# Kernel optimization log

Measured on AMD Instinct MI355X. Metric: run time of the kernel, lower is better.

Reference implementation:

```python
import jax, jax.numpy as jnp
import numpy as np

N = 100000   # nodes
D = 64       # padded neighbor-list width (avg degree)
F = 256      # in_channels
H = 256      # hidden_channels
E = 131072   # number of target edges
OUT = 1      # out_channels


def _linear_params(key, fin, fout):
    k1, k2 = jax.random.split(key)
    s = 1.0 / np.sqrt(fin)
    w = jax.random.uniform(k1, (fin, fout), jnp.float32, -s, s)
    b = jax.random.uniform(k2, (fout,), jnp.float32, -s, s)
    return w, b


def setup_inputs() -> dict:
    key = jax.random.key(0)
    ks = jax.random.split(key, 12)
    x = jax.random.normal(ks[0], (N, F), jnp.float32)
    # sorted padded neighbor lists: row i -> D neighbor ids (sorted, as in the
    # bit-packed sorted-element representation the torch code intersects)
    neighbors = jnp.sort(jax.random.randint(ks[1], (N, D), 0, N), axis=1).astype(jnp.int32)
    tar_ei = jax.random.randint(ks[2], (2, E), 0, N).astype(jnp.int32)
    cn_w1, cn_b1 = _linear_params(ks[3], 1, H)
    cn_w2, cn_b2 = _linear_params(ks[4], H, H)
    cn_w3, cn_b3 = _linear_params(ks[5], H, H)
    ij_w1, ij_b1 = _linear_params(ks[6], F, H)
    ij_w2, ij_b2 = _linear_params(ks[7], H, H)
    lin_w1, lin_b1 = _linear_params(ks[8], H, H)
    lin_w2, lin_b2 = _linear_params(ks[9], H, OUT)
    beta = jnp.ones((1,), jnp.float32)
    return dict(x=x, neighbors=neighbors, tar_ei=tar_ei, beta=beta,
                cn_w1=cn_w1, cn_b1=cn_b1, cn_w2=cn_w2, cn_b2=cn_b2,
                cn_w3=cn_w3, cn_b3=cn_b3,
                ij_w1=ij_w1, ij_b1=ij_b1, ij_w2=ij_w2, ij_b2=ij_b2,
                lin_w1=lin_w1, lin_b1=lin_b1, lin_w2=lin_w2, lin_b2=lin_b2)


def reference(x, neighbors, tar_ei, beta,
              cn_w1, cn_b1, cn_w2, cn_b2, cn_w3, cn_b3,
              ij_w1, ij_b1, ij_w2, ij_b2,
              lin_w1, lin_b1, lin_w2, lin_b2):
    src, dst = tar_ei[0], tar_ei[1]
    xi = x[src]                       # [E, F] irregular gather
    xj = x[dst]                       # [E, F]

    # adjoverlap / spmoverlap_: per edge, |N(i) ∩ N(j)| via sorted-set
    # intersection; cn.sum(dim=-1) with fill value 1.0 -> CN count.
    ni = neighbors[src]               # [E, D]
    nj = neighbors[dst]               # [E, D]
    matches = ni[:, :, None] == nj[:, None, :]          # [E, D, D]
    xcn = jnp.sum(matches, axis=(1, 2)).astype(jnp.float32)[:, None]  # [E, 1]

    # xcnlin: Linear(1,H) -> ReLU -> Linear(H,H) -> ReLU -> Linear(H,H)
    h = jax.nn.relu(xcn @ cn_w1 + cn_b1)
    h = jax.nn.relu(h @ cn_w2 + cn_b2)
    xcn_feat = h @ cn_w3 + cn_b3                         # [E, H]

    # xijlin: Linear(F,H) -> ReLU -> Linear(H,H)
    g = jax.nn.relu((xi * xj) @ ij_w1 + ij_b1)
    xij = g @ ij_w2 + ij_b2                              # [E, H]

    # lin: Linear(H,H) -> ReLU -> Linear(H,OUT)
    z = jax.nn.relu((xcn_feat * beta + xij) @ lin_w1 + lin_b1)
    out = z @ lin_w2 + lin_b2                            # [E, OUT]
    return out
```

## Files before the change

### kernel.cpp

```cpp
#include <hip/hip_runtime.h>
#include <hip/hip_bf16.h>
#include <stdint.h>

#define EE 131072
#define DDEG 64

typedef __bf16 bf16_t;
typedef bf16_t bf16x8 __attribute__((ext_vector_type(8)));
typedef float floatx4 __attribute__((ext_vector_type(4)));

__global__ __launch_bounds__(256)
void cn_kernel(const int* __restrict__ nbr, const int* __restrict__ tar,
               int* __restrict__ xcn) {
    int wid  = (blockIdx.x * 256 + threadIdx.x) >> 6;
    int lane = threadIdx.x & 63;
    int s = __builtin_amdgcn_readfirstlane(tar[wid]);
    int d = __builtin_amdgcn_readfirstlane(tar[EE + wid]);
    int a = nbr[(size_t)s * DDEG + lane];
    const int* __restrict__ brow = nbr + (size_t)d * DDEG;
    int cnt = 0;
    #pragma unroll
    for (int k = 0; k < 64; ++k)
        cnt += __builtin_popcountll(__ballot(a == brow[k]));
    if (lane == 0) xcn[wid] = cnt;
}

__global__ __launch_bounds__(256)
void prep_kernel(const float* __restrict__ x, bf16_t* __restrict__ xb,
                 const float* __restrict__ ij_w1, bf16_t* __restrict__ Wt1,
                 const float* __restrict__ w2, const float* __restrict__ lw1,
                 bf16_t* __restrict__ Mt,
                 const float* __restrict__ b2, const float* __restrict__ lb1,
                 float* __restrict__ cvec,
                 const float* __restrict__ cw1, const float* __restrict__ cb1,
                 const float* __restrict__ cw2, const float* __restrict__ cb2,
                 const float* __restrict__ cw3, const float* __restrict__ cb3,
                 const float* __restrict__ beta, float* __restrict__ T2) {
    __shared__ __align__(16) char arena[33792];
    const int bid = blockIdx.x;
    const int t = threadIdx.x;

    if (bid >= 1088) {
        size_t base = (size_t)(bid - 1088) * 4096 + (size_t)t * 16;
        float4 a0 = *(const float4*)(x + base);
        float4 a1 = *(const float4*)(x + base + 4);
        float4 a2 = *(const float4*)(x + base + 8);
        float4 a3 = *(const float4*)(x + base + 12);
        bf16x8 o0, o1;
        o0[0] = (bf16_t)a0.x; o0[1] = (bf16_t)a0.y; o0[2] = (bf16_t)a0.z; o0[3] = (bf16_t)a0.w;
        o0[4] = (bf16_t)a1.x; o0[5] = (bf16_t)a1.y; o0[6] = (bf16_t)a1.z; o0[7] = (bf16_t)a1.w;
        o1[0] = (bf16_t)a2.x; o1[1] = (bf16_t)a2.y; o1[2] = (bf16_t)a2.z; o1[3] = (bf16_t)a2.w;
        o1[4] = (bf16_t)a3.x; o1[5] = (bf16_t)a3.y; o1[6] = (bf16_t)a3.z; o1[7] = (bf16_t)a3.w;
        *(bf16x8*)(xb + base)     = o0;
        *(bf16x8*)(xb + base + 8) = o1;
        return;
    }

    if (bid < 64) {
        float (*tile)[33] = (float (*)[33])arena;
        int bx = bid & 7, by = bid >> 3;
        int tx = t & 31, ty = t >> 5;
        #pragma unroll
        for (int r = 0; r < 32; r += 8)
            tile[ty + r][tx] = ij_w1[(by * 32 + ty + r) * 256 + bx * 32 + tx];
        __syncthreads();
        #pragma unroll
        for (int r = 0; r < 32; r += 8)
            Wt1[(bx * 32 + ty + r) * 256 + by * 32 + tx] = (bf16_t)tile[tx][ty + r];
    } else if (bid < 320) {
        float (*S)[33] = (float (*)[33])arena;
        int b = bid - 64;
        int cc = t & 31, abase = t >> 5;
        float acc = 0.f;
        for (int c0 = 0; c0 < 256; c0 += 32) {
            __syncthreads();
            #pragma unroll
            for (int r = 0; r < 32; ++r) {
                int a = r * 8 + abase;
                S[a][cc] = w2[a * 256 + c0 + cc];
            }
            __syncthreads();
            #pragma unroll 8
            for (int c2 = 0; c2 < 32; ++c2) {
                float wv = lw1[(c0 + c2) * 256 + b];
                acc += S[t][c2] * wv;
            }
        }
        Mt[(size_t)b * 256 + t] = (bf16_t)acc;
    } else if (bid < 576) {
        float* red = (float*)arena;
        int b = bid - 320;
        red[t] = b2[t] * lw1[t * 256 + b];
        __syncthreads();
        for (int s = 128; s > 0; s >>= 1) {
            if (t < s) red[t] += red[t + s];
            __syncthreads();
        }
        if (t == 0) cvec[b] = red[0] + lb1[b];
    } else {
        float* t1 = (float*)arena;
        float* t2 = (float*)(arena + 1024);
        float* t3 = (float*)(arena + 2048);
        int v = bid - 576;
        float fv = (float)v;
        t1[t] = fmaxf(fv * cw1[t] + cb1[t], 0.f);
        __syncthreads();
        float s = cb2[t];
        for (int k = 0; k < 256; ++k) s += t1[k] * cw2[k * 256 + t];
        t2[t] = fmaxf(s, 0.f);
        __syncthreads();
        s = cb3[t];
        for (int k = 0; k < 256; ++k) s += t2[k] * cw3[k * 256 + t];
        t3[t] = s * beta[0];
        __syncthreads();
        s = 0.f;
        for (int k = 0; k < 256; ++k) s += t3[k] * lw1[k * 256 + t];
        T2[(size_t)v * 256 + t] = s;
    }
}

__global__ __launch_bounds__(256, 4)
void fused_kernel(const bf16_t* __restrict__ xb, const int* __restrict__ tar,
                  const bf16_t* __restrict__ Wt1, const float* __restrict__ b1,
                  const bf16_t* __restrict__ Mt, const float* __restrict__ cvec,
                  const float* __restrict__ T2, const int* __restrict__ xcn,
                  const float* __restrict__ w2, const float* __restrict__ b2s,
                  float* __restrict__ out) {
    __shared__ __align__(16) bf16_t X[64 * 264];
    __shared__ float rowacc[64];

    const int tid  = threadIdx.x;
    const int lane = tid & 63;
    const int wc   = tid >> 6;
    const int quad = lane >> 4;
    const int l16  = lane & 15;
    const int e0   = blockIdx.x * 64;

    {
        const int srow   = tid >> 2;
        const int skbase = (tid & 3) * 8;
        int e = e0 + srow;
        const bf16_t* xi = xb + (size_t)tar[e] * 256 + skbase;
        const bf16_t* xj = xb + (size_t)tar[EE + e] * 256 + skbase;
        bf16x8 ui[8], vj[8];
        #pragma unroll
        for (int kc = 0; kc < 8; ++kc) {
            ui[kc] = *(const bf16x8*)(xi + kc * 32);
            vj[kc] = *(const bf16x8*)(xj + kc * 32);
        }
        #pragma unroll
        for (int kc = 0; kc < 8; ++kc) {
            bf16x8 p;
            #pragma unroll
            for (int m = 0; m < 8; ++m)
                p[m] = (bf16_t)((float)ui[kc][m] * (float)vj[kc][m]);
            *(bf16x8*)&X[srow * 264 + kc * 32 + skbase] = p;
        }
    }

    floatx4 acc[4][4];
    #pragma unroll
    for (int i = 0; i < 4; ++i)
        #pragma unroll
        for (int j = 0; j < 4; ++j)
            acc[i][j] = (floatx4){0.f, 0.f, 0.f, 0.f};

    __syncthreads();

    #pragma unroll 2
    for (int kc = 0; kc < 8; ++kc) {
        const int k0 = kc * 32 + quad * 8;
        bf16x8 af[4], bfr[4];
        #pragma unroll
        for (int j = 0; j < 4; ++j)
            bfr[j] = *(const bf16x8*)(Wt1 + (size_t)(wc * 64 + j * 16 + l16) * 256 + k0);
        #pragma unroll
        for (int i = 0; i < 4; ++i)
            af[i] = *(const bf16x8*)(&X[(i * 16 + l16) * 264 + k0]);
        #pragma unroll
        for (int i = 0; i < 4; ++i)
            #pragma unroll
            for (int j = 0; j < 4; ++j)
                acc[i][j] = __builtin_amdgcn_mfma_f32_16x16x32_bf16(
                                af[i], bfr[j], acc[i][j], 0, 0, 0);
    }

    __syncthreads();

    #pragma unroll
    for (int j = 0; j < 4; ++j) {
        int col  = wc * 64 + j * 16 + l16;
        float bv = b1[col];
        #pragma unroll
        for (int i = 0; i < 4; ++i)
            #pragma unroll
            for (int r = 0; r < 4; ++r) {
                int row = i * 16 + quad * 4 + r;
                X[row * 264 + col] = (bf16_t)fmaxf(acc[i][j][r] + bv, 0.f);
            }
    }
    #pragma unroll
    for (int i = 0; i < 4; ++i)
        #pragma unroll
        for (int j = 0; j < 4; ++j)
            acc[i][j] = (floatx4){0.f, 0.f, 0.f, 0.f};
    if (tid < 64) rowacc[tid] = 0.f;

    __syncthreads();

    #pragma unroll 2
    for (int kc = 0; kc < 8; ++kc) {
        const int k0 = kc * 32 + quad * 8;
        bf16x8 af[4], bfr[4];
        #pragma unroll
        for (int j = 0; j < 4; ++j)
            bfr[j] = *(const bf16x8*)(Mt + (size_t)(wc * 64 + j * 16 + l16) * 256 + k0);
        #pragma unroll
        for (int i = 0; i < 4; ++i)
            af[i] = *(const bf16x8*)(&X[(i * 16 + l16) * 264 + k0]);
        #pragma unroll
        for (int i = 0; i < 4; ++i)
            #pragma unroll
            for (int j = 0; j < 4; ++j)
                acc[i][j] = __builtin_amdgcn_mfma_f32_16x16x32_bf16(
                                af[i], bfr[j], acc[i][j], 0, 0, 0);
    }

    int xv[16];
    #pragma unroll
    for (int i = 0; i < 4; ++i)
        #pragma unroll
        for (int r = 0; r < 4; ++r) {
            int v = xcn[e0 + i * 16 + quad * 4 + r];
            xv[i * 4 + r] = v < 511 ? v : 511;
        }

    float pr[16];
    #pragma unroll
    for (int t = 0; t < 16; ++t) pr[t] = 0.f;
    #pragma unroll
    for (int j = 0; j < 4; ++j) {
        int col  = wc * 64 + j * 16 + l16;
        float cv = cvec[col];
        float wv = w2[col];
        #pragma unroll
        for (int i = 0; i < 4; ++i)
            #pragma unroll
            for (int r = 0; r < 4; ++r) {
                float t2v = T2[(size_t)xv[i * 4 + r] * 256 + col];
                float v = fmaxf(acc[i][j][r] + cv + t2v, 0.f);
                pr[i * 4 + r] += v * wv;
            }
    }
    #pragma unroll
    for (int off = 1; off < 16; off <<= 1)
        #pragma unroll
        for (int t = 0; t < 16; ++t)
            pr[t] += __shfl_xor(pr[t], off, 64);
    if (l16 == 0) {
        #pragma unroll
        for (int i = 0; i < 4; ++i)
            #pragma unroll
            for (int r = 0; r < 4; ++r)
                atomicAdd(&rowacc[i * 16 + quad * 4 + r], pr[i * 4 + r]);
    }
    __syncthreads();
    if (tid < 64) out[e0 + tid] = rowacc[tid] + b2s[0];
}

extern "C" void kernel_launch(void* const* d_in, const int* in_sizes, int n_in,
                              void* d_out, int out_size, void* d_ws, size_t ws_size,
                              hipStream_t stream) {
    const float* x      = (const float*)d_in[0];
    const int*   nbr    = (const int*)  d_in[1];
    const int*   tar    = (const int*)  d_in[2];
    const float* beta   = (const float*)d_in[3];
    const float* cn_w1  = (const float*)d_in[4];
    const float* cn_b1  = (const float*)d_in[5];
    const float* cn_w2  = (const float*)d_in[6];
    const float* cn_b2  = (const float*)d_in[7];
    const float* cn_w3  = (const float*)d_in[8];
    const float* cn_b3  = (const float*)d_in[9];
    const float* ij_w1  = (const float*)d_in[10];
    const float* ij_b1  = (const float*)d_in[11];
    const float* ij_w2  = (const float*)d_in[12];
    const float* ij_b2  = (const float*)d_in[13];
    const float* lin_w1 = (const float*)d_in[14];
    const float* lin_b1 = (const float*)d_in[15];
    const float* lin_w2 = (const float*)d_in[16];
    const float* lin_b2 = (const float*)d_in[17];

    char* ws = (char*)d_ws;
    float*  T2    = (float*) (ws + 0);
    int*    xcn   = (int*)   (ws + 524288);
    bf16_t* Wt1   = (bf16_t*)(ws + 1048576);
    bf16_t* Mt    = (bf16_t*)(ws + 1179648);
    float*  cvec  = (float*) (ws + 1310720);
    bf16_t* xb    = (bf16_t*)(ws + 1312768);

    cn_kernel<<<EE / 4, 256, 0, stream>>>(nbr, tar, xcn);
    prep_kernel<<<1088 + 6250, 256, 0, stream>>>(
        x, xb, ij_w1, Wt1, ij_w2, lin_w1, Mt,
        ij_b2, lin_b1, cvec,
        cn_w1, cn_b1, cn_w2, cn_b2, cn_w3, cn_b3, beta, T2);
    fused_kernel<<<EE / 64, 256, 0, stream>>>(xb, tar, Wt1, ij_b1, Mt, cvec,
                                              T2, xcn, lin_w2, lin_b2,
                                              (float*)d_out);
}
```

Baseline: 371.0 us.

## Fuse common-neighbor count into MLP kernel with binary-search intersection and swizzled LDS

Removes the separate cn_kernel and computes the common-neighbor count inside the fused MLP kernel, dropping a global round trip for xcn and one launch. The count now uses a per-lane binary search over shuffled sorted neighbor lists (lower/upper bound) in place of 64 ballots. The edge tile shrinks from 64 to 32 rows per block and occupancy is raised to 6 blocks. LDS padding is replaced by an XOR swizzle to avoid bank conflicts. Smaller tiles mean the weight fragments (Wt1, Mt) are reloaded from memory twice as often per edge.

```diff
diff --git a/kernel.cpp b/kernel.cpp
--- a/kernel.cpp
+++ b/kernel.cpp
@@ -9,21 +9,7 @@
 typedef bf16_t bf16x8 __attribute__((ext_vector_type(8)));
 typedef float floatx4 __attribute__((ext_vector_type(4)));
 
-__global__ __launch_bounds__(256)
-void cn_kernel(const int* __restrict__ nbr, const int* __restrict__ tar,
-               int* __restrict__ xcn) {
-    int wid  = (blockIdx.x * 256 + threadIdx.x) >> 6;
-    int lane = threadIdx.x & 63;
-    int s = __builtin_amdgcn_readfirstlane(tar[wid]);
-    int d = __builtin_amdgcn_readfirstlane(tar[EE + wid]);
-    int a = nbr[(size_t)s * DDEG + lane];
-    const int* __restrict__ brow = nbr + (size_t)d * DDEG;
-    int cnt = 0;
-    #pragma unroll
-    for (int k = 0; k < 64; ++k)
-        cnt += __builtin_popcountll(__ballot(a == brow[k]));
-    if (lane == 0) xcn[wid] = cnt;
-}
+#define SWZ(row, k) (((row) << 8) + ((k) ^ (((row) & 7) << 3)))
 
 __global__ __launch_bounds__(256)
 void prep_kernel(const float* __restrict__ x, bf16_t* __restrict__ xb,
@@ -119,48 +105,77 @@
     }
 }
 
-__global__ __launch_bounds__(256, 4)
+__global__ __launch_bounds__(256, 6)
 void fused_kernel(const bf16_t* __restrict__ xb, const int* __restrict__ tar,
+                  const int* __restrict__ nbr,
                   const bf16_t* __restrict__ Wt1, const float* __restrict__ b1,
                   const bf16_t* __restrict__ Mt, const float* __restrict__ cvec,
-                  const float* __restrict__ T2, const int* __restrict__ xcn,
+                  const float* __restrict__ T2,
                   const float* __restrict__ w2, const float* __restrict__ b2s,
                   float* __restrict__ out) {
-    __shared__ __align__(16) bf16_t X[64 * 264];
-    __shared__ float rowacc[64];
+    __shared__ __align__(16) bf16_t X[32 * 256];
+    __shared__ float rowacc[32];
+    __shared__ int xcn_s[32];
 
     const int tid  = threadIdx.x;
     const int lane = tid & 63;
     const int wc   = tid >> 6;
     const int quad = lane >> 4;
     const int l16  = lane & 15;
-    const int e0   = blockIdx.x * 64;
+    const int e0   = blockIdx.x * 32;
 
     {
-        const int srow   = tid >> 2;
-        const int skbase = (tid & 3) * 8;
+        const int srow   = tid >> 3;
+        const int skbase = (tid & 7) * 8;
         int e = e0 + srow;
         const bf16_t* xi = xb + (size_t)tar[e] * 256 + skbase;
         const bf16_t* xj = xb + (size_t)tar[EE + e] * 256 + skbase;
-        bf16x8 ui[8], vj[8];
-        #pragma unroll
-        for (int kc = 0; kc < 8; ++kc) {
-            ui[kc] = *(const bf16x8*)(xi + kc * 32);
-            vj[kc] = *(const bf16x8*)(xj + kc * 32);
-        }
-        #pragma unroll
-        for (int kc = 0; kc < 8; ++kc) {
+        bf16x8 ui[4], vj[4];
+        #pragma unroll
+        for (int kc = 0; kc < 4; ++kc) {
+            ui[kc] = *(const bf16x8*)(xi + kc * 64);
+            vj[kc] = *(const bf16x8*)(xj + kc * 64);
+        }
+        #pragma unroll
+        for (int kc = 0; kc < 4; ++kc) {
             bf16x8 p;
             #pragma unroll
             for (int m = 0; m < 8; ++m)
                 p[m] = (bf16_t)((float)ui[kc][m] * (float)vj[kc][m]);
-            *(bf16x8*)&X[srow * 264 + kc * 32 + skbase] = p;
-        }
-    }
-
-    floatx4 acc[4][4];
-    #pragma unroll
-    for (int i = 0; i < 4; ++i)
+            *(bf16x8*)&X[SWZ(srow, kc * 64 + skbase)] = p;
+        }
+    }
+
+    #pragma unroll 2
+    for (int i = 0; i < 8; ++i) {
+        int e = e0 + wc * 8 + i;
+        int s = __builtin_amdgcn_readfirstlane(tar[e]);
+        int d = __builtin_amdgcn_readfirstlane(tar[EE + e]);
+        int va = nbr[(size_t)s * DDEG + lane];
+        int vb = nbr[(size_t)d * DDEG + lane];
+        int lo = 0, hi = 0;
+        #pragma unroll
+        for (int st = 32; st; st >>= 1) {
+            int bv = __shfl(vb, lo + st - 1, 64);
+            lo += (bv < va) ? st : 0;
+        }
+        #pragma unroll
+        for (int st = 32; st; st >>= 1) {
+            int bv = __shfl(vb, hi + st - 1, 64);
+            hi += (bv <= va) ? st : 0;
+        }
+        int b63 = __shfl(vb, 63, 64);
+        lo += (b63 < va) ? 1 : 0;
+        hi += (b63 <= va) ? 1 : 0;
+        int c = hi - lo;
+        #pragma unroll
+        for (int off = 32; off; off >>= 1) c += __shfl_xor(c, off, 64);
+        if (lane == 0) xcn_s[wc * 8 + i] = (c < 511) ? c : 511;
+    }
+
+    floatx4 acc[2][4];
+    #pragma unroll
+    for (int i = 0; i < 2; ++i)
         #pragma unroll
         for (int j = 0; j < 4; ++j)
             acc[i][j] = (floatx4){0.f, 0.f, 0.f, 0.f};
@@ -170,15 +185,17 @@
     #pragma unroll 2
     for (int kc = 0; kc < 8; ++kc) {
         const int k0 = kc * 32 + quad * 8;
-        bf16x8 af[4], bfr[4];
+        bf16x8 af[2], bfr[4];
         #pragma unroll
         for (int j = 0; j < 4; ++j)
             bfr[j] = *(const bf16x8*)(Wt1 + (size_t)(wc * 64 + j * 16 + l16) * 256 + k0);
         #pragma unroll
-        for (int i = 0; i < 4; ++i)
-            af[i] = *(const bf16x8*)(&X[(i * 16 + l16) * 264 + k0]);
-        #pragma unroll
-        for (int i = 0; i < 4; ++i)
+        for (int i = 0; i < 2; ++i) {
+            int row = i * 16 + l16;
+            af[i] = *(const bf16x8*)(&X[SWZ(row, k0)]);
+        }
+        #pragma unroll
+        for (int i = 0; i < 2; ++i)
             #pragma unroll
             for (int j = 0; j < 4; ++j)
                 acc[i][j] = __builtin_amdgcn_mfma_f32_16x16x32_bf16(
@@ -192,59 +209,59 @@
         int col  = wc * 64 + j * 16 + l16;
         float bv = b1[col];
         #pragma unroll
-        for (int i = 0; i < 4; ++i)
+        for (int i = 0; i < 2; ++i)
             #pragma unroll
             for (int r = 0; r < 4; ++r) {
                 int row = i * 16 + quad * 4 + r;
-                X[row * 264 + col] = (bf16_t)fmaxf(acc[i][j][r] + bv, 0.f);
+                X[SWZ(row, col)] = (bf16_t)fmaxf(acc[i][j][r] + bv, 0.f);
             }
     }
     #pragma unroll
-    for (int i = 0; i < 4; ++i)
+    for (int i = 0; i < 2; ++i)
         #pragma unroll
         for (int j = 0; j < 4; ++j)
             acc[i][j] = (floatx4){0.f, 0.f, 0.f, 0.f};
-    if (tid < 64) rowacc[tid] = 0.f;
+    if (tid < 32) rowacc[tid] = 0.f;
 
     __syncthreads();
 
     #pragma unroll 2
     for (int kc = 0; kc < 8; ++kc) {
         const int k0 = kc * 32 + quad * 8;
-        bf16x8 af[4], bfr[4];
+        bf16x8 af[2], bfr[4];
         #pragma unroll
         for (int j = 0; j < 4; ++j)
             bfr[j] = *(const bf16x8*)(Mt + (size_t)(wc * 64 + j * 16 + l16) * 256 + k0);
         #pragma unroll
-        for (int i = 0; i < 4; ++i)
-            af[i] = *(const bf16x8*)(&X[(i * 16 + l16) * 264 + k0]);
-        #pragma unroll
-        for (int i = 0; i < 4; ++i)
+        for (int i = 0; i < 2; ++i) {
+            int row = i * 16 + l16;
+            af[i] = *(const bf16x8*)(&X[SWZ(row, k0)]);
+        }
+        #pragma unroll
+        for (int i = 0; i < 2; ++i)
             #pragma unroll
             for (int j = 0; j < 4; ++j)
                 acc[i][j] = __builtin_amdgcn_mfma_f32_16x16x32_bf16(
                                 af[i], bfr[j], acc[i][j], 0, 0, 0);
     }
 
-    int xv[16];
-    #pragma unroll
-    for (int i = 0; i < 4; ++i)
-        #pragma unroll
-        for (int r = 0; r < 4; ++r) {
-            int v = xcn[e0 + i * 16 + quad * 4 + r];
-            xv[i * 4 + r] = v < 511 ? v : 511;
-        }
-
-    float pr[16];
-    #pragma unroll
-    for (int t = 0; t < 16; ++t) pr[t] = 0.f;
+    int xv[8];
+    #pragma unroll
+    for (int i = 0; i < 2; ++i)
+        #pragma unroll
+        for (int r = 0; r < 4; ++r)
+            xv[i * 4 + r] = xcn_s[i * 16 + quad * 4 + r];
+
+    float pr[8];
+    #pragma unroll
+    for (int t = 0; t < 8; ++t) pr[t] = 0.f;
     #pragma unroll
     for (int j = 0; j < 4; ++j) {
         int col  = wc * 64 + j * 16 + l16;
         float cv = cvec[col];
         float wv = w2[col];
         #pragma unroll
-        for (int i = 0; i < 4; ++i)
+        for (int i = 0; i < 2; ++i)
             #pragma unroll
             for (int r = 0; r < 4; ++r) {
                 float t2v = T2[(size_t)xv[i * 4 + r] * 256 + col];
@@ -255,17 +272,17 @@
     #pragma unroll
     for (int off = 1; off < 16; off <<= 1)
         #pragma unroll
-        for (int t = 0; t < 16; ++t)
+        for (int t = 0; t < 8; ++t)
             pr[t] += __shfl_xor(pr[t], off, 64);
     if (l16 == 0) {
         #pragma unroll
-        for (int i = 0; i < 4; ++i)
+        for (int i = 0; i < 2; ++i)
             #pragma unroll
             for (int r = 0; r < 4; ++r)
                 atomicAdd(&rowacc[i * 16 + quad * 4 + r], pr[i * 4 + r]);
     }
     __syncthreads();
-    if (tid < 64) out[e0 + tid] = rowacc[tid] + b2s[0];
+    if (tid < 32) out[e0 + tid] = rowacc[tid] + b2s[0];
 }
 
 extern "C" void kernel_launch(void* const* d_in, const int* in_sizes, int n_in,
@@ -292,18 +309,16 @@
 
     char* ws = (char*)d_ws;
     float*  T2    = (float*) (ws + 0);
-    int*    xcn   = (int*)   (ws + 524288);
     bf16_t* Wt1   = (bf16_t*)(ws + 1048576);
     bf16_t* Mt    = (bf16_t*)(ws + 1179648);
     float*  cvec  = (float*) (ws + 1310720);
     bf16_t* xb    = (bf16_t*)(ws + 1312768);
 
-    cn_kernel<<<EE / 4, 256, 0, stream>>>(nbr, tar, xcn);
     prep_kernel<<<1088 + 6250, 256, 0, stream>>>(
         x, xb, ij_w1, Wt1, ij_w2, lin_w1, Mt,
         ij_b2, lin_b1, cvec,
         cn_w1, cn_b1, cn_w2, cn_b2, cn_w3, cn_b3, beta, T2);
-    fused_kernel<<<EE / 64, 256, 0, stream>>>(xb, tar, Wt1, ij_b1, Mt, cvec,
-                                              T2, xcn, lin_w2, lin_b2,
+    fused_kernel<<<EE / 32, 256, 0, stream>>>(xb, tar, nbr, Wt1, ij_b1, Mt, cvec,
+                                              T2, lin_w2, lin_b2,
                                               (float*)d_out);
 }
```

New measurement: 389.3 us. 4.9% more time.

## Fuse common-neighbor counting into main kernel via binary-search intersection and swizzle LDS

Applied to the files above, without the earlier changes.

Removes the separate cn_kernel and computes per-edge common-neighbor counts inside fused_kernel. Each wave loads both neighbor rows and counts matches per element with a shuffle-based binary search over the sorted partner row, replacing 64 ballots. Counts are packed two per int for the reduction and stored in LDS. The X tile drops its padding and uses an XOR swizzle to avoid bank conflicts. Launch bounds go from 4 to 3 blocks per CU, since the 32 extra registers holding neighbor rows raise register pressure and lower occupancy.

```diff
diff --git a/kernel.cpp b/kernel.cpp
--- a/kernel.cpp
+++ b/kernel.cpp
@@ -9,21 +9,7 @@
 typedef bf16_t bf16x8 __attribute__((ext_vector_type(8)));
 typedef float floatx4 __attribute__((ext_vector_type(4)));
 
-__global__ __launch_bounds__(256)
-void cn_kernel(const int* __restrict__ nbr, const int* __restrict__ tar,
-               int* __restrict__ xcn) {
-    int wid  = (blockIdx.x * 256 + threadIdx.x) >> 6;
-    int lane = threadIdx.x & 63;
-    int s = __builtin_amdgcn_readfirstlane(tar[wid]);
-    int d = __builtin_amdgcn_readfirstlane(tar[EE + wid]);
-    int a = nbr[(size_t)s * DDEG + lane];
-    const int* __restrict__ brow = nbr + (size_t)d * DDEG;
-    int cnt = 0;
-    #pragma unroll
-    for (int k = 0; k < 64; ++k)
-        cnt += __builtin_popcountll(__ballot(a == brow[k]));
-    if (lane == 0) xcn[wid] = cnt;
-}
+#define SWZ(row, k) (((row) << 8) + ((k) ^ (((row) & 7) << 3)))
 
 __global__ __launch_bounds__(256)
 void prep_kernel(const float* __restrict__ x, bf16_t* __restrict__ xb,
@@ -119,15 +105,17 @@
     }
 }
 
-__global__ __launch_bounds__(256, 4)
+__global__ __launch_bounds__(256, 3)
 void fused_kernel(const bf16_t* __restrict__ xb, const int* __restrict__ tar,
+                  const int* __restrict__ nbr,
                   const bf16_t* __restrict__ Wt1, const float* __restrict__ b1,
                   const bf16_t* __restrict__ Mt, const float* __restrict__ cvec,
-                  const float* __restrict__ T2, const int* __restrict__ xcn,
+                  const float* __restrict__ T2,
                   const float* __restrict__ w2, const float* __restrict__ b2s,
                   float* __restrict__ out) {
-    __shared__ __align__(16) bf16_t X[64 * 264];
+    __shared__ __align__(16) bf16_t X[64 * 256];
     __shared__ float rowacc[64];
+    __shared__ int xcn_s[64];
 
     const int tid  = threadIdx.x;
     const int lane = tid & 63;
@@ -135,6 +123,16 @@
     const int quad = lane >> 4;
     const int l16  = lane & 15;
     const int e0   = blockIdx.x * 64;
+
+    int va[16], vb[16];
+    #pragma unroll
+    for (int i = 0; i < 16; ++i) {
+        int e = e0 + wc * 16 + i;
+        int s = __builtin_amdgcn_readfirstlane(tar[e]);
+        int d = __builtin_amdgcn_readfirstlane(tar[EE + e]);
+        va[i] = nbr[(size_t)s * DDEG + lane];
+        vb[i] = nbr[(size_t)d * DDEG + lane];
+    }
 
     {
         const int srow   = tid >> 2;
@@ -154,7 +152,37 @@
             #pragma unroll
             for (int m = 0; m < 8; ++m)
                 p[m] = (bf16_t)((float)ui[kc][m] * (float)vj[kc][m]);
-            *(bf16x8*)&X[srow * 264 + kc * 32 + skbase] = p;
+            *(bf16x8*)&X[SWZ(srow, kc * 32 + skbase)] = p;
+        }
+    }
+
+    __syncthreads();
+
+    #pragma unroll
+    for (int p = 0; p < 8; ++p) {
+        int cpk = 0;
+        #pragma unroll
+        for (int h = 0; h < 2; ++h) {
+            int i = p * 2 + h;
+            int lo = 0, hi = 0;
+            #pragma unroll
+            for (int st = 32; st; st >>= 1) {
+                int bl = __shfl(vb[i], lo + st - 1, 64);
+                int bh = __shfl(vb[i], hi + st - 1, 64);
+                lo += (bl < va[i]) ? st : 0;
+                hi += (bh <= va[i]) ? st : 0;
+            }
+            int b63 = __shfl(vb[i], 63, 64);
+            lo += (b63 < va[i]) ? 1 : 0;
+            hi += (b63 <= va[i]) ? 1 : 0;
+            cpk += (hi - lo) << (16 * h);
+        }
+        #pragma unroll
+        for (int off = 32; off; off >>= 1) cpk += __shfl_xor(cpk, off, 64);
+        if (lane == 0) {
+            int c0 = cpk & 0xffff, c1 = (int)((unsigned)cpk >> 16);
+            xcn_s[wc * 16 + p * 2]     = c0 < 511 ? c0 : 511;
+            xcn_s[wc * 16 + p * 2 + 1] = c1 < 511 ? c1 : 511;
         }
     }
 
@@ -164,8 +192,6 @@
         #pragma unroll
         for (int j = 0; j < 4; ++j)
             acc[i][j] = (floatx4){0.f, 0.f, 0.f, 0.f};
-
-    __syncthreads();
 
     #pragma unroll 2
     for (int kc = 0; kc < 8; ++kc) {
@@ -176,7 +202,7 @@
             bfr[j] = *(const bf16x8*)(Wt1 + (size_t)(wc * 64 + j * 16 + l16) * 256 + k0);
         #pragma unroll
         for (int i = 0; i < 4; ++i)
-            af[i] = *(const bf16x8*)(&X[(i * 16 + l16) * 264 + k0]);
+            af[i] = *(const bf16x8*)(&X[SWZ(i * 16 + l16, k0)]);
         #pragma unroll
         for (int i = 0; i < 4; ++i)
             #pragma unroll
@@ -196,7 +222,7 @@
             #pragma unroll
             for (int r = 0; r < 4; ++r) {
                 int row = i * 16 + quad * 4 + r;
-                X[row * 264 + col] = (bf16_t)fmaxf(acc[i][j][r] + bv, 0.f);
+                X[SWZ(row, col)] = (bf16_t)fmaxf(acc[i][j][r] + bv, 0.f);
             }
     }
     #pragma unroll
@@ -217,7 +243,7 @@
             bfr[j] = *(const bf16x8*)(Mt + (size_t)(wc * 64 + j * 16 + l16) * 256 + k0);
         #pragma unroll
         for (int i = 0; i < 4; ++i)
-            af[i] = *(const bf16x8*)(&X[(i * 16 + l16) * 264 + k0]);
+            af[i] = *(const bf16x8*)(&X[SWZ(i * 16 + l16, k0)]);
         #pragma unroll
         for (int i = 0; i < 4; ++i)
             #pragma unroll
@@ -230,10 +256,8 @@
     #pragma unroll
     for (int i = 0; i < 4; ++i)
         #pragma unroll
-        for (int r = 0; r < 4; ++r) {
-            int v = xcn[e0 + i * 16 + quad * 4 + r];
-            xv[i * 4 + r] = v < 511 ? v : 511;
-        }
+        for (int r = 0; r < 4; ++r)
+            xv[i * 4 + r] = xcn_s[i * 16 + quad * 4 + r];
 
     float pr[16];
     #pragma unroll
@@ -292,18 +316,16 @@
 
     char* ws = (char*)d_ws;
     float*  T2    = (float*) (ws + 0);
-    int*    xcn   = (int*)   (ws + 524288);
     bf16_t* Wt1   = (bf16_t*)(ws + 1048576);
     bf16_t* Mt    = (bf16_t*)(ws + 1179648);
     float*  cvec  = (float*) (ws + 1310720);
     bf16_t* xb    = (bf16_t*)(ws + 1312768);
 
-    cn_kernel<<<EE / 4, 256, 0, stream>>>(nbr, tar, xcn);
     prep_kernel<<<1088 + 6250, 256, 0, stream>>>(
         x, xb, ij_w1, Wt1, ij_w2, lin_w1, Mt,
         ij_b2, lin_b1, cvec,
         cn_w1, cn_b1, cn_w2, cn_b2, cn_w3, cn_b3, beta, T2);
-    fused_kernel<<<EE / 64, 256, 0, stream>>>(xb, tar, Wt1, ij_b1, Mt, cvec,
-                                              T2, xcn, lin_w2, lin_b2,
+    fused_kernel<<<EE / 64, 256, 0, stream>>>(xb, tar, nbr, Wt1, ij_b1, Mt, cvec,
+                                              T2, lin_w2, lin_b2,
                                               (float*)d_out);
 }
```

Measured after the change: 313.3 us, median of 2. -15.6%, faster.
